# Kernel optimization log

Measured on AMD Instinct MI355X. Metric: run time of the kernel, lower is better.

## Reference

```python
import jax, jax.numpy as jnp
import numpy as np

C1, C2, C3, S = 3, 6, 3, 16
SPLITS = (9 * C1 * 1, C1, 9 * C2 * C1, C2, 9 * C3 * C2, C3, 9 * S * C3, S)  # sums to 811
B = 16384


def _channelize(w, cin, cout):
    # w: [B, cout*9*cin] -> filter [3, 3, cin, B*cout] (B-major on out axis)
    w = w.reshape(-1, cout, 9 * cin)
    w = jnp.transpose(w, (2, 0, 1))          # [9*cin, B, cout]
    return w.reshape(3, 3, cin, -1)


def _gconv(x, w, groups):
    # x: [1, H, W, B*cin], w: [3, 3, cin, B*cout]; grouped conv, groups=B
    return jax.lax.conv_general_dilated(
        x, w, window_strides=(1, 1), padding='VALID',
        dimension_numbers=('NHWC', 'HWIO', 'NHWC'),
        feature_group_count=groups)


def _maxpool2(x):
    return jax.lax.reduce_window(x, -jnp.inf, jax.lax.max,
                                 (1, 2, 2, 1), (1, 2, 2, 1), 'VALID')


def setup_inputs() -> dict:
    key = jax.random.key(0)
    ks = jax.random.split(key, 8)
    tot = sum(SPLITS)
    return {
        'image': jax.random.normal(ks[0], (1, 28, 28, B), jnp.float32),
        'state': jax.random.normal(ks[1], (B, S), jnp.float32),
        'W1': jax.random.normal(ks[2], (S, 16), jnp.float32) * 0.25,
        'b1': jnp.zeros((16,), jnp.float32),
        'W2': jax.random.normal(ks[3], (16, 16), jnp.float32) * 0.25,
        'b2': jnp.zeros((16,), jnp.float32),
        'W3': jax.random.normal(ks[4], (16, tot), jnp.float32) * 0.1,
        'b3': jnp.zeros((tot,), jnp.float32),
    }


def reference(image, state, W1, b1, W2, b2, W3, b3):
    batch = state.shape[0]
    # Hypernetwork MLP producing per-sample conv weights (dropout rate 0 => identity)
    h = jax.nn.relu(state @ W1 + b1)
    h = jax.nn.relu(h @ W2 + b2)
    w = h @ W3 + b3                               # [B, 811]
    idx = np.cumsum(SPLITS)[:-1]
    w1, bb1, w2, bb2, w3, bb3, w4, bb4 = jnp.split(w, idx, axis=1)

    x = _gconv(image, _channelize(w1, 1, C1), batch) + bb1.reshape(-1)   # [1,26,26,B*C1]
    x = _maxpool2(jax.nn.relu(x))                                        # [1,13,13,B*C1]
    x = _gconv(x, _channelize(w2, C1, C2), batch) + bb2.reshape(-1)      # [1,11,11,B*C2]
    x = _maxpool2(jax.nn.relu(x))                                        # [1,5,5,B*C2]
    x = _gconv(x, _channelize(w3, C2, C3), batch) + bb3.reshape(-1)      # [1,3,3,B*C3]
    x = jax.nn.relu(x)
    x = _gconv(x, _channelize(w4, C3, S), batch) + bb4.reshape(-1)       # [1,1,1,B*S]
    x = jnp.transpose(x, (3, 1, 2, 0)).reshape(-1, S)                    # [B, S]
    return state + x
```

## Files before the change

### kernel.cpp

```cpp
#include <hip/hip_runtime.h>

#define BLK   512
#define NSAMP 8
#define REG   1480
#define OFF_P2   0
#define OFF_P3   152
#define OFF_W    392
#define HW_P1    2408
#define DW_P1    1204


__device__ __forceinline__ float bf2f(unsigned short u) {
    return __uint_as_float(((unsigned int)u) << 16);
}
__device__ __forceinline__ unsigned short f2bf(float f) {
    unsigned int x = __float_as_uint(f);
    return (unsigned short)((x + 0x7fffu + ((x >> 16) & 1u)) >> 16);
}
__device__ __forceinline__ void wsync() {
    __builtin_amdgcn_wave_barrier();
    __asm__ volatile("s_waitcnt lgkmcnt(0)" ::: "memory");
    __builtin_amdgcn_wave_barrier();
}

__device__ __forceinline__ bool is_bf16(const void* p, int elems) {
    const unsigned short* h = (const unsigned short*)p;
    int n = elems; if (n > 32) n = 32;
    int nz = 0, ok = 0;
    for (int i = 0; i < n; i += 2) {
        unsigned short u = h[i];
        if (u == 0) continue;
        ++nz;
        unsigned int e = (u >> 7) & 255u;
        if (e >= 100u && e <= 141u) ++ok;
    }
    if (nz < 4) return true;
    return 4 * ok >= 3 * nz;
}

__global__ __launch_bounds__(BLK, 4)
void dyncnn4_kernel(const void* __restrict__ image,
                    const void* __restrict__ state,
                    const void* __restrict__ W1, const void* __restrict__ b1,
                    const void* __restrict__ W2, const void* __restrict__ b2,
                    const void* __restrict__ W3, const void* __restrict__ b3,
                    void* __restrict__ out,
                    int B, int nswz)
{
    __shared__ float SH[NSAMP * REG];
    __shared__ float s_st[NSAMP][16];
    __shared__ float s_h1[NSAMP][16];
    __shared__ float s_h2[NSAMP][16];
    __shared__ unsigned char s_fl[8];

    const int t    = threadIdx.x;
    const int wv   = t >> 6;
    const int lane = t & 63;

    if (t < 8) {
        const void* q; int n;
        switch (t) {
            case 0:  q = image; n = 784 * B; break;
            case 1:  q = state; n = 16 * B;  break;
            case 2:  q = W1;    n = 256;     break;
            case 3:  q = b1;    n = 16;      break;
            case 4:  q = W2;    n = 256;     break;
            case 5:  q = b2;    n = 16;      break;
            case 6:  q = W3;    n = 12976;   break;
            default: q = b3;    n = 811;     break;
        }
        s_fl[t] = is_bf16(q, n) ? 1 : 0;
    }
    __syncthreads();
    const bool im_bf = s_fl[0], st_bf = s_fl[1], w1_bf = s_fl[2], b1_bf = s_fl[3];
    const bool w2_bf = s_fl[4], b2_bf = s_fl[5], w3_bf = s_fl[6], b3_bf = s_fl[7];
    const bool out_bf = im_bf && st_bf && w1_bf && w2_bf && w3_bf;

    int p = blockIdx.x;
    int l = (nswz > 0) ? ((p & 7) * nswz + (p >> 3)) : p;
    const int b0 = l * NSAMP;

    unsigned short* su = (unsigned short*)SH;

    if (wv < 2) {
        int s = wv * 4 + (lane >> 4), j = lane & 15;
        int gi = (b0 + s) * 16 + j;
        s_st[s][j] = st_bf ? bf2f(((const unsigned short*)state)[gi])
                           : ((const float*)state)[gi];
        wsync();
        float acc = b1_bf ? bf2f(((const unsigned short*)b1)[j])
                          : ((const float*)b1)[j];
#pragma unroll
        for (int k = 0; k < 16; ++k) {
            float w = w1_bf ? bf2f(((const unsigned short*)W1)[k * 16 + j])
                            : ((const float*)W1)[k * 16 + j];
            acc += s_st[s][k] * w;
        }
        s_h1[s][j] = fmaxf(acc, 0.f);
        wsync();
        acc = b2_bf ? bf2f(((const unsigned short*)b2)[j])
                    : ((const float*)b2)[j];
#pragma unroll
        for (int k = 0; k < 16; ++k) {
            float w = w2_bf ? bf2f(((const unsigned short*)W2)[k * 16 + j])
                            : ((const float*)W2)[k * 16 + j];
            acc += s_h1[s][k] * w;
        }
        s_h2[s][j] = fmaxf(acc, 0.f);
    } else {
        if (im_bf) {
            const unsigned short* im = (const unsigned short*)image;
            for (int pix = t - 128; pix < 784; pix += 384) {
                const uint4 v = *(const uint4*)(im + pix * B + b0);
                su[0 * 2 * REG + pix] = (unsigned short)(v.x);
                su[1 * 2 * REG + pix] = (unsigned short)(v.x >> 16);
                su[2 * 2 * REG + pix] = (unsigned short)(v.y);
                su[3 * 2 * REG + pix] = (unsigned short)(v.y >> 16);
                su[4 * 2 * REG + pix] = (unsigned short)(v.z);
                su[5 * 2 * REG + pix] = (unsigned short)(v.z >> 16);
                su[6 * 2 * REG + pix] = (unsigned short)(v.w);
                su[7 * 2 * REG + pix] = (unsigned short)(v.w >> 16);
            }
        } else {
            const float* im = (const float*)image;
            for (int pix = t - 128; pix < 784; pix += 384) {
                const float4 a = *(const float4*)(im + pix * B + b0);
                const float4 c = *(const float4*)(im + pix * B + b0 + 4);
                su[0 * 2 * REG + pix] = f2bf(a.x);
                su[1 * 2 * REG + pix] = f2bf(a.y);
                su[2 * 2 * REG + pix] = f2bf(a.z);
                su[3 * 2 * REG + pix] = f2bf(a.w);
                su[4 * 2 * REG + pix] = f2bf(c.x);
                su[5 * 2 * REG + pix] = f2bf(c.y);
                su[6 * 2 * REG + pix] = f2bf(c.z);
                su[7 * 2 * REG + pix] = f2bf(c.w);
            }
        }
    }
    __syncthreads();

#pragma unroll
    for (int sp = 0; sp < NSAMP; sp += 2) {
        float h2a[16], h2b[16];
#pragma unroll
        for (int k = 0; k < 16; ++k) { h2a[k] = s_h2[sp][k]; h2b[k] = s_h2[sp + 1][k]; }
        for (int j = t; j < 811; j += BLK) {
            float bb = b3_bf ? bf2f(((const unsigned short*)b3)[j])
                             : ((const float*)b3)[j];
            float aa = bb, ab = bb;
            if (w3_bf) {
                const unsigned short* q = (const unsigned short*)W3 + j;
#pragma unroll
                for (int k = 0; k < 16; ++k) {
                    float w = bf2f(q[k * 811]);
                    aa += h2a[k] * w; ab += h2b[k] * w;
                }
            } else {
                const float* q = (const float*)W3 + j;
#pragma unroll
                for (int k = 0; k < 16; ++k) {
                    float w = q[k * 811];
                    aa += h2a[k] * w; ab += h2b[k] * w;
                }
            }
            SH[sp * REG + OFF_W + j]       = aa;
            SH[(sp + 1) * REG + OFF_W + j] = ab;
        }
    }
    __syncthreads();

    const int sb  = wv * REG;
    const int sb2 = wv * 2 * REG;

    {
        float wc[27], cb[3];
#pragma unroll
        for (int i = 0; i < 27; ++i) wc[i] = SH[sb + OFF_W + i];
#pragma unroll
        for (int c = 0; c < 3; ++c) cb[c] = SH[sb + OFF_W + 27 + c];
        const unsigned* suw = (const unsigned*)&SH[sb];
#pragma unroll
        for (int it = 0; it < 3; ++it) {
            int pix = lane + it * 64;
            if (pix < 169) {
                int py = pix / 13, px = pix - py * 13;
                int iy = 2 * py;
                float pt[4][4];
#pragma unroll
                for (int dy = 0; dy < 4; ++dy) {
                    int r = (iy + dy) * 14 + px;
                    unsigned d0 = suw[r], d1 = suw[r + 1];
                    pt[dy][0] = __uint_as_float(d0 << 16);
                    pt[dy][1] = __uint_as_float(d0 & 0xffff0000u);
                    pt[dy][2] = __uint_as_float(d1 << 16);
                    pt[dy][3] = __uint_as_float(d1 & 0xffff0000u);
                }
                unsigned short* op = &su[sb2 + HW_P1 + py * 14 + px];
#pragma unroll
                for (int c = 0; c < 3; ++c) {
                    float a00 = 0.f, a01 = 0.f, a10 = 0.f, a11 = 0.f;
#pragma unroll
                    for (int ky = 0; ky < 3; ++ky)
#pragma unroll
                        for (int kx = 0; kx < 3; ++kx) {
                            float w = wc[c * 9 + ky * 3 + kx];
                            a00 += pt[ky][kx] * w;
                            a01 += pt[ky][kx + 1] * w;
                            a10 += pt[ky + 1][kx] * w;
                            a11 += pt[ky + 1][kx + 1] * w;
                        }
                    float m = fmaxf(fmaxf(a00, a01), fmaxf(a10, a11));
                    op[c * 182] = f2bf(fmaxf(m + cb[c], 0.f));
                }
            }
        }
    }
    wsync();

    {
        int g = lane >> 5, q = lane & 31;
        if (q < 25) {
            int py = q / 5, px = q - py * 5;
            const unsigned* p1w = (const unsigned*)&SH[sb + DW_P1];
            float acc[3][4];
#pragma unroll
            for (int it = 0; it < 3; ++it)
#pragma unroll
                for (int i = 0; i < 4; ++i) acc[it][i] = 0.f;
#pragma unroll
            for (int ci = 0; ci < 3; ++ci) {
                float pt[4][4];
#pragma unroll
                for (int dy = 0; dy < 4; ++dy) {
                    int r = ci * 91 + (2 * py + dy) * 7 + px;
                    unsigned d0 = p1w[r], d1 = p1w[r + 1];
                    pt[dy][0] = __uint_as_float(d0 << 16);
                    pt[dy][1] = __uint_as_float(d0 & 0xffff0000u);
                    pt[dy][2] = __uint_as_float(d1 << 16);
                    pt[dy][3] = __uint_as_float(d1 & 0xffff0000u);
                }
#pragma unroll
                for (int it = 0; it < 3; ++it) {
                    int c = it * 2 + g;
                    const int wo = sb + OFF_W + 30 + c * 27 + ci;
#pragma unroll
                    for (int ky = 0; ky < 3; ++ky)
#pragma unroll
                        for (int kx = 0; kx < 3; ++kx) {
                            float w = SH[wo + (ky * 3 + kx) * 3];
                            acc[it][0] += pt[ky][kx] * w;
                            acc[it][1] += pt[ky][kx + 1] * w;
                            acc[it][2] += pt[ky + 1][kx] * w;
                            acc[it][3] += pt[ky + 1][kx + 1] * w;
                        }
                }
            }
#pragma unroll
            for (int it = 0; it < 3; ++it) {
                int c = it * 2 + g;
                float m = fmaxf(fmaxf(acc[it][0], acc[it][1]),
                                fmaxf(acc[it][2], acc[it][3]));
                SH[sb + OFF_P2 + c * 25 + q] =
                    fmaxf(m + SH[sb + OFF_W + 192 + c], 0.f);
            }
        }
    }
    wsync();

    {
        float acc = 0.f;
        int pq = lane % 27;
        int half = lane / 27;
        int c = pq / 9, pos = pq - c * 9;
        int py = pos / 3, px = pos - py * 3;
        if (lane < 54) {
            const int wo = sb + OFF_W + 198 + c * 54;
            const int cb3 = half * 3;
#pragma unroll
            for (int ky = 0; ky < 3; ++ky)
#pragma unroll
                for (int kx = 0; kx < 3; ++kx)
#pragma unroll
                    for (int ci = 0; ci < 3; ++ci)
                        acc += SH[sb + OFF_P2 + (cb3 + ci) * 25 + (py + ky) * 5 + px + kx] *
                               SH[wo + (ky * 3 + kx) * 6 + cb3 + ci];
        }
        float other = __shfl(acc, (lane + 27) & 63);
        if (lane < 27)
            SH[sb + OFF_P3 + pq] =
                fmaxf(acc + other + SH[sb + OFF_W + 360 + c], 0.f);
    }
    wsync();

    {
        float acc = 0.f;
        int os = lane & 15, h = (lane >> 4) & 1;
        if (lane < 32) {
            const int wo = sb + OFF_W + 363 + os * 27;
            int p0 = h ? 4 : 0, p1 = h ? 9 : 4;
            for (int pp = p0; pp < p1; ++pp)
#pragma unroll
                for (int ci = 0; ci < 3; ++ci)
                    acc += SH[sb + OFF_P3 + ci * 9 + pp] * SH[wo + pp * 3 + ci];
        }
        float other = __shfl(acc, (lane + 16) & 63);
        if (lane < 16) {
            float tot = acc + other + SH[sb + OFF_W + 795 + os] + s_st[wv][os];
            int gi = (b0 + wv) * 16 + os;
            if (out_bf) ((unsigned short*)out)[gi] = f2bf(tot);
            else        ((float*)out)[gi] = tot;
        }
    }
}

extern "C" void kernel_launch(void* const* d_in, const int* in_sizes, int n_in,
                              void* d_out, int out_size, void* d_ws, size_t ws_size,
                              hipStream_t stream) {
    (void)d_ws; (void)ws_size; (void)n_in; (void)out_size;
    int B = in_sizes[1] / 16;
    int nblocks = B / NSAMP;
    int nswz = (nblocks % 8 == 0) ? (nblocks / 8) : 0;

    dyncnn4_kernel<<<nblocks, BLK, 0, stream>>>(
        d_in[0], d_in[1], d_in[2], d_in[3], d_in[4], d_in[5], d_in[6], d_in[7],
        d_out, B, nswz);
}
```

Baseline: 149.0 us.

## Compute hypernetwork output layer with bf16 MFMA and unroll image load loop

Replaces the scalar per-thread FMA loop for the final hypernetwork layer (h2 @ W3 + b3, producing 811 weights per sample for 8 samples) with a 16x16x32 bf16 MFMA per 16-column tile, distributed across the 8 waves. The A fragment holds the hidden activations (8 samples by 16 K, zero padded) and the B fragment holds W3 columns. Activations and fp32 weights are rounded to bf16, which loses precision compared with the fp32 accumulation path. The bf16 image-load loop is also manually unrolled so the loads are issued together before the LDS stores.

```diff
diff --git a/kernel.cpp b/kernel.cpp
--- a/kernel.cpp
+++ b/kernel.cpp
@@ -9,6 +9,9 @@
 #define HW_P1    2408
 #define DW_P1    1204
 
+
+typedef short bf16x8 __attribute__((ext_vector_type(8)));
+typedef float f32x4  __attribute__((ext_vector_type(4)));
 
 __device__ __forceinline__ float bf2f(unsigned short u) {
     return __uint_as_float(((unsigned int)u) << 16);
@@ -108,10 +111,17 @@
         }
         s_h2[s][j] = fmaxf(acc, 0.f);
     } else {
+        int pix0 = t - 128;
+        int pix1 = pix0 + 384;
+        int pix2 = pix0 + 768;
         if (im_bf) {
             const unsigned short* im = (const unsigned short*)image;
-            for (int pix = t - 128; pix < 784; pix += 384) {
-                const uint4 v = *(const uint4*)(im + pix * B + b0);
+            const uint4 v0 = *(const uint4*)(im + pix0 * B + b0);
+            const uint4 v1 = *(const uint4*)(im + pix1 * B + b0);
+#pragma unroll
+            for (int h = 0; h < 2; ++h) {
+                const uint4 v = h ? v1 : v0;
+                int pix = h ? pix1 : pix0;
                 su[0 * 2 * REG + pix] = (unsigned short)(v.x);
                 su[1 * 2 * REG + pix] = (unsigned short)(v.x >> 16);
                 su[2 * 2 * REG + pix] = (unsigned short)(v.y);
@@ -121,9 +131,20 @@
                 su[6 * 2 * REG + pix] = (unsigned short)(v.w);
                 su[7 * 2 * REG + pix] = (unsigned short)(v.w >> 16);
             }
+            if (pix2 < 784) {
+                const uint4 v = *(const uint4*)(im + pix2 * B + b0);
+                su[0 * 2 * REG + pix2] = (unsigned short)(v.x);
+                su[1 * 2 * REG + pix2] = (unsigned short)(v.x >> 16);
+                su[2 * 2 * REG + pix2] = (unsigned short)(v.y);
+                su[3 * 2 * REG + pix2] = (unsigned short)(v.y >> 16);
+                su[4 * 2 * REG + pix2] = (unsigned short)(v.z);
+                su[5 * 2 * REG + pix2] = (unsigned short)(v.z >> 16);
+                su[6 * 2 * REG + pix2] = (unsigned short)(v.w);
+                su[7 * 2 * REG + pix2] = (unsigned short)(v.w >> 16);
+            }
         } else {
             const float* im = (const float*)image;
-            for (int pix = t - 128; pix < 784; pix += 384) {
+            for (int pix = pix0; pix < 784; pix += 384) {
                 const float4 a = *(const float4*)(im + pix * B + b0);
                 const float4 c = *(const float4*)(im + pix * B + b0 + 4);
                 su[0 * 2 * REG + pix] = f2bf(a.x);
@@ -139,32 +160,45 @@
     }
     __syncthreads();
 
-#pragma unroll
-    for (int sp = 0; sp < NSAMP; sp += 2) {
-        float h2a[16], h2b[16];
-#pragma unroll
-        for (int k = 0; k < 16; ++k) { h2a[k] = s_h2[sp][k]; h2b[k] = s_h2[sp + 1][k]; }
-        for (int j = t; j < 811; j += BLK) {
-            float bb = b3_bf ? bf2f(((const unsigned short*)b3)[j])
-                             : ((const float*)b3)[j];
-            float aa = bb, ab = bb;
-            if (w3_bf) {
-                const unsigned short* q = (const unsigned short*)W3 + j;
-#pragma unroll
-                for (int k = 0; k < 16; ++k) {
-                    float w = bf2f(q[k * 811]);
-                    aa += h2a[k] * w; ab += h2b[k] * w;
-                }
-            } else {
-                const float* q = (const float*)W3 + j;
-#pragma unroll
-                for (int k = 0; k < 16; ++k) {
-                    float w = q[k * 811];
-                    aa += h2a[k] * w; ab += h2b[k] * w;
-                }
-            }
-            SH[sp * REG + OFF_W + j]       = aa;
-            SH[(sp + 1) * REG + OFF_W + j] = ab;
+    {
+        const int n  = lane & 15;
+        const int kg = lane >> 4;
+        bf16x8 afrag;
+#pragma unroll
+        for (int i = 0; i < 8; ++i) afrag[i] = 0;
+        if (kg < 2 && n < 8) {
+            const int k0 = kg * 8;
+#pragma unroll
+            for (int i = 0; i < 8; ++i)
+                afrag[i] = (short)f2bf(s_h2[n][k0 + i]);
+        }
+        for (int tile = wv; tile < 51; tile += 8) {
+            const int jn = tile * 16 + n;
+            bf16x8 bfrag;
+#pragma unroll
+            for (int i = 0; i < 8; ++i) bfrag[i] = 0;
+            if (kg < 2 && jn < 811) {
+                const int k0 = kg * 8;
+                if (w3_bf) {
+                    const unsigned short* q = (const unsigned short*)W3 + k0 * 811 + jn;
+#pragma unroll
+                    for (int i = 0; i < 8; ++i) bfrag[i] = (short)q[i * 811];
+                } else {
+                    const float* q = (const float*)W3 + k0 * 811 + jn;
+#pragma unroll
+                    for (int i = 0; i < 8; ++i) bfrag[i] = (short)f2bf(q[i * 811]);
+                }
+            }
+            f32x4 c = {0.f, 0.f, 0.f, 0.f};
+            c = __builtin_amdgcn_mfma_f32_16x16x32_bf16(afrag, bfrag, c, 0, 0, 0);
+            const int row0 = kg * 4;
+            if (row0 < 8 && jn < 811) {
+                float bb = b3_bf ? bf2f(((const unsigned short*)b3)[jn])
+                                 : ((const float*)b3)[jn];
+#pragma unroll
+                for (int r = 0; r < 4; ++r)
+                    SH[(row0 + r) * REG + OFF_W + jn] = c[r] + bb;
+            }
         }
     }
     __syncthreads();
```

Result: faster. 142.7 us (-4.3%).
